# Kernel optimization log

Measured on AMD Instinct MI355X. Metric: run time of the kernel, lower is better.

Reference implementation:

```python
import jax, jax.numpy as jnp
import numpy as np

B, T, C, H = 2, 2048, 1024, 16
D = C // H  # head dim = 64
EPS = 1e-5


def setup_inputs() -> dict:
    key = jax.random.key(0)
    k1, k2, k3 = jax.random.split(key, 3)
    x = jax.random.normal(k1, (B, T, C), dtype=jnp.float32)
    W_attn = jax.random.normal(k2, (3 * C, C), dtype=jnp.float32) * 0.02
    W_proj = jax.random.normal(k3, (C, C), dtype=jnp.float32) * 0.02
    # standard RoPE inverse frequencies, one per rotation pair (D//2)
    rope_freqs = 1.0 / (10000.0 ** (jnp.arange(D // 2, dtype=jnp.float32) * 2.0 / D))
    ln_weight = jnp.ones((C,), dtype=jnp.float32)
    ln_bias = jnp.zeros((C,), dtype=jnp.float32)
    return {"x": x, "rope_freqs": rope_freqs, "W_attn": W_attn,
            "W_proj": W_proj, "ln_weight": ln_weight, "ln_bias": ln_bias}


def _apply_rope(q, k, freqs):
    # q,k: [B,H,S,D]; matches torch apply_rope: split even/odd, concat halves
    S = q.shape[-2]
    theta = jnp.arange(S, dtype=q.dtype)[:, None] * freqs[None, :]  # [S, D/2]
    sin_t, cos_t = jnp.sin(theta), jnp.cos(theta)

    def rot(t):
        t1, t2 = t[..., 0::2], t[..., 1::2]
        return jnp.concatenate([t1 * cos_t - t2 * sin_t,
                                t1 * sin_t + t2 * cos_t], axis=-1)

    return rot(q), rot(k)


def reference(x, rope_freqs, W_attn, W_proj, ln_weight, ln_bias):
    Bv, Tv, Cv = x.shape
    qkv = x @ W_attn.T                      # [B,T,3C] (F.linear, no bias)
    q, k, v = jnp.split(qkv, 3, axis=-1)
    resh = lambda t: t.reshape(Bv, Tv, H, D).transpose(0, 2, 1, 3)  # [B,H,T,D]
    q, k, v = resh(q), resh(k), resh(v)
    q, k = _apply_rope(q, k, rope_freqs)
    scale = 1.0 / jnp.sqrt(jnp.asarray(D, dtype=x.dtype))
    scores = jnp.einsum('bhqd,bhkd->bhqk', q, k) * scale
    causal = jnp.tril(jnp.ones((Tv, Tv), dtype=bool))
    scores = jnp.where(causal[None, None], scores, -jnp.inf)
    att = jax.nn.softmax(scores, axis=-1)
    y = jnp.einsum('bhqk,bhkd->bhqd', att, v)
    y = y.transpose(0, 2, 1, 3).reshape(Bv, Tv, Cv)
    y = y @ W_proj.T                        # c_proj (bias=False)
    # resid dropout is identity in eval; LayerNorm (eps=1e-5, biased var)
    mean = jnp.mean(y, axis=-1, keepdims=True)
    var = jnp.mean(jnp.square(y - mean), axis=-1, keepdims=True)
    return (y - mean) / jnp.sqrt(var + EPS) * ln_weight + ln_bias
```

## Files before the change

kernel.cpp:

```cpp
#include <hip/hip_runtime.h>
#include <hip/hip_bf16.h>
#include <math.h>

typedef short bf16x8 __attribute__((ext_vector_type(8)));
typedef float f32x4 __attribute__((ext_vector_type(4)));

#define T_SEQ 2048
#define C_DIM 1024
#define H_HEADS 16
#define D_HEAD 64
#define BT 4096
#define C3 3072
#define BH 32

static __device__ inline unsigned short bf_bits(float f) {
    __hip_bfloat16 h = __float2bfloat16(f);
    unsigned short u;
    __builtin_memcpy(&u, &h, 2);
    return u;
}

static __device__ inline unsigned int cvtpk(float lo, float hi) {
    unsigned int r;
    asm("v_cvt_pk_bf16_f32 %0, %1, %2" : "=v"(r) : "v"(lo), "v"(hi));
    return r;
}

__device__ __forceinline__ void gload16(const void* g, void* l) {
    __builtin_amdgcn_global_load_lds(
        (const __attribute__((address_space(1))) void*)g,
        (__attribute__((address_space(3))) void*)l, 16, 0, 0);
}

__device__ __forceinline__ int swz(int r) {
    return ((((r & 3) ^ ((r >> 3) & 3)) | (((r >> 3) & 1) << 2)) << 3);
}

__global__ void cast_f32_bf16(const float* __restrict__ in,
                              __hip_bfloat16* __restrict__ out, int n4) {
    int i = blockIdx.x * blockDim.x + threadIdx.x;
    if (i >= n4) return;
    float4 v = reinterpret_cast<const float4*>(in)[i];
    ushort4 o;
    o.x = bf_bits(v.x); o.y = bf_bits(v.y); o.z = bf_bits(v.z); o.w = bf_bits(v.w);
    reinterpret_cast<ushort4*>(out)[i] = o;
}

template<int OUT_BF16>
__global__ __launch_bounds__(256) void gemm_bt(
    const __hip_bfloat16* __restrict__ A,
    const __hip_bfloat16* __restrict__ Bw,
    void* __restrict__ Cout, int M, int N, int K) {
    __shared__ __hip_bfloat16 As[2][128][64];
    __shared__ __hip_bfloat16 Bs[2][128][64];
    const int t = threadIdx.x;
    const int lane = t & 63, w = t >> 6;
    const int wr = w >> 1, wc = w & 1;
    const int l15 = lane & 15, lg = lane >> 4;
    const int m0 = blockIdx.y * 128, n0 = blockIdx.x * 128;

    const int srow = lane >> 3;
    const int scol = ((lane & 7) ^ srow) * 8;
    const int xr = (l15 & 7) << 3;

    f32x4 acc[4][4];
    f32x4 zero4 = {0.f, 0.f, 0.f, 0.f};
#pragma unroll
    for (int m = 0; m < 4; m++)
#pragma unroll
        for (int n = 0; n < 4; n++) acc[m][n] = zero4;

    auto stage = [&](int buf, int k0) {
#pragma unroll
        for (int i = 0; i < 4; i++) {
            int rbase = w * 32 + i * 8;
            gload16(&A[(size_t)(m0 + rbase + srow) * K + k0 + scol], &As[buf][rbase][0]);
            gload16(&Bw[(size_t)(n0 + rbase + srow) * K + k0 + scol], &Bs[buf][rbase][0]);
        }
    };

    const int nt = K >> 6;
    stage(0, 0);
    __syncthreads();

    for (int tk = 0; tk < nt; tk++) {
        const int cur = tk & 1;
        if (tk + 1 < nt) stage(cur ^ 1, (tk + 1) << 6);
#pragma unroll
        for (int kk = 0; kk < 2; kk++) {
            bf16x8 a[4], b[4];
            const int co = (kk * 32 + lg * 8) ^ xr;
#pragma unroll
            for (int m = 0; m < 4; m++)
                a[m] = *reinterpret_cast<const bf16x8*>(&As[cur][wr * 64 + m * 16 + l15][co]);
#pragma unroll
            for (int n = 0; n < 4; n++)
                b[n] = *reinterpret_cast<const bf16x8*>(&Bs[cur][wc * 64 + n * 16 + l15][co]);
            __builtin_amdgcn_s_setprio(1);
#pragma unroll
            for (int m = 0; m < 4; m++)
#pragma unroll
                for (int n = 0; n < 4; n++)
                    acc[m][n] = __builtin_amdgcn_mfma_f32_16x16x32_bf16(a[m], b[n], acc[m][n], 0, 0, 0);
            __builtin_amdgcn_s_setprio(0);
        }
        __syncthreads();
    }

#pragma unroll
    for (int m = 0; m < 4; m++)
#pragma unroll
        for (int n = 0; n < 4; n++)
#pragma unroll
            for (int jj = 0; jj < 4; jj++) {
                int row = m0 + wr * 64 + m * 16 + lg * 4 + jj;
                int col = n0 + wc * 64 + n * 16 + l15;
                float v = acc[m][n][jj];
                if (OUT_BF16)
                    ((__hip_bfloat16*)Cout)[(size_t)row * N + col] = __float2bfloat16(v);
                else
                    ((float*)Cout)[(size_t)row * N + col] = v;
            }
}

__global__ void rope_qk(const __hip_bfloat16* __restrict__ qkv,
                        const float* __restrict__ freqs,
                        __hip_bfloat16* __restrict__ q_s,
                        __hip_bfloat16* __restrict__ k_s) {
    int idx = blockIdx.x * 256 + threadIdx.x;
    int i = idx & 31;
    int h = (idx >> 5) & 15;
    int bt = idx >> 9;
    int b = bt >> 11;
    int tp = bt & 2047;
    float th = (float)tp * freqs[i];
    float sn = sinf(th), cs = cosf(th);
    size_t qoff = (size_t)bt * C3 + h * 64;
    float q1 = __bfloat162float(qkv[qoff + 2 * i]);
    float q2 = __bfloat162float(qkv[qoff + 2 * i + 1]);
    float k1 = __bfloat162float(qkv[qoff + C_DIM + 2 * i]);
    float k2 = __bfloat162float(qkv[qoff + C_DIM + 2 * i + 1]);
    size_t obase = ((size_t)(b * H_HEADS + h) * T_SEQ + tp) * D_HEAD;
    const float sc = 0.125f * 1.44269504f;
    q_s[obase + i]      = __float2bfloat16((q1 * cs - q2 * sn) * sc);
    q_s[obase + 32 + i] = __float2bfloat16((q1 * sn + q2 * cs) * sc);
    k_s[obase + i]      = __float2bfloat16(k1 * cs - k2 * sn);
    k_s[obase + 32 + i] = __float2bfloat16(k1 * sn + k2 * cs);
}

__global__ __launch_bounds__(256) void transpose_v(const __hip_bfloat16* __restrict__ qkv,
                                                   __hip_bfloat16* __restrict__ v_t) {
    __shared__ __hip_bfloat16 tile[64][72];
    const int bh = blockIdx.y, tt = blockIdx.x;
    const int b = bh >> 4, h = bh & 15;
    const int t = threadIdx.x;
    const int r = t >> 2, c0 = (t & 3) * 16;
    const __hip_bfloat16* src = qkv + (size_t)(b * T_SEQ + tt * 64 + r) * C3 + 2 * C_DIM + h * 64 + c0;
    uint4 v0 = reinterpret_cast<const uint4*>(src)[0];
    uint4 v1 = reinterpret_cast<const uint4*>(src)[1];
    *reinterpret_cast<uint4*>(&tile[r][c0]) = v0;
    *reinterpret_cast<uint4*>(&tile[r][c0 + 8]) = v1;
    __syncthreads();
    const int d = t >> 2;
    ushort out[16];
#pragma unroll
    for (int i = 0; i < 16; i++) {
        __hip_bfloat16 x = tile[c0 + i][d];
        __builtin_memcpy(&out[i], &x, 2);
    }
    __hip_bfloat16* dst = v_t + (size_t)bh * D_HEAD * T_SEQ + (size_t)d * T_SEQ + tt * 64 + c0;
    reinterpret_cast<uint4*>(dst)[0] = *reinterpret_cast<uint4*>(&out[0]);
    reinterpret_cast<uint4*>(dst)[1] = *reinterpret_cast<uint4*>(&out[8]);
}

__global__ __launch_bounds__(256, 4) void attn_kernel(
    const __hip_bfloat16* __restrict__ q_s,
    const __hip_bfloat16* __restrict__ k_s,
    const __hip_bfloat16* __restrict__ v_t,
    __hip_bfloat16* __restrict__ y) {
    __shared__ ushort Kbuf[2][64 * 64];
    __shared__ ushort Vbuf[2][64 * 64];

    const int bid = blockIdx.x;
    const int qt = 31 - (bid >> 5);
    const int bh = bid & 31;
    const int t = threadIdx.x, lane = t & 63, w = t >> 6;
    const int l15 = lane & 15, lg = lane >> 4;
    const size_t hbase = (size_t)bh * T_SEQ * D_HEAD;
    const int qr = qt * 64 + w * 16 + l15;

    bf16x8 aq[2];
#pragma unroll
    for (int dd = 0; dd < 2; dd++)
        aq[dd] = *reinterpret_cast<const bf16x8*>(&q_s[hbase + (size_t)qr * 64 + dd * 32 + lg * 8]);

    bf16x8 ones;
#pragma unroll
    for (int i = 0; i < 8; i++) ones[i] = (short)0x3F80;

    f32x4 zero4 = {0.f, 0.f, 0.f, 0.f};
    f32x4 o[4];
#pragma unroll
    for (int dc = 0; dc < 4; dc++) o[dc] = zero4;
    f32x4 lacc = zero4;
    float mr = -INFINITY;

    int koff[4][2], voff[4][2];
#pragma unroll
    for (int c = 0; c < 4; c++) {
        int kro = ((c >> 1) << 5) + ((c & 1) << 2) + ((l15 >> 2) << 3) + (l15 & 3);
        int sz = swz(kro);
#pragma unroll
        for (int dd = 0; dd < 2; dd++)
            koff[c][dd] = kro * 64 + ((dd * 32 + lg * 8) ^ sz);
    }
#pragma unroll
    for (int dc = 0; dc < 4; dc++) {
        int vro = dc * 16 + l15;
        int sz = swz(vro);
#pragma unroll
        for (int dd = 0; dd < 2; dd++)
            voff[dc][dd] = vro * 64 + ((dd * 32 + lg * 8) ^ sz);
    }

    const int srow = t >> 3;
    const int sgr = t & 7;

    auto stageKV = [&](int buf, int kbase) {
#pragma unroll
        for (int i = 0; i < 2; i++) {
            int r = i * 32 + srow;
            int gsw = (sgr ^ (swz(r) >> 3)) * 8;
            gload16(&k_s[hbase + (size_t)(kbase + r) * 64 + gsw],
                    &Kbuf[buf][(i * 32 + w * 8) * 64]);
            gload16(&v_t[hbase + (size_t)r * T_SEQ + kbase + gsw],
                    &Vbuf[buf][(i * 32 + w * 8) * 64]);
        }
    };

    int cur = 0;
    stageKV(0, 0);
    __syncthreads();

    for (int kt = 0; kt <= qt; kt++) {
        const int kt64 = kt << 6;
        if (kt < qt) stageKV(cur ^ 1, kt64 + 64);

        const ushort* Kc = Kbuf[cur];
        const ushort* Vc = Vbuf[cur];
        bf16x8 kf[4][2], av[4][2];
#pragma unroll
        for (int c = 0; c < 4; c++)
#pragma unroll
            for (int dd = 0; dd < 2; dd++)
                kf[c][dd] = *reinterpret_cast<const bf16x8*>(&Kc[koff[c][dd]]);
#pragma unroll
        for (int dc = 0; dc < 4; dc++)
#pragma unroll
            for (int dd = 0; dd < 2; dd++)
                av[dc][dd] = *reinterpret_cast<const bf16x8*>(&Vc[voff[dc][dd]]);

        f32x4 st[4];
        __builtin_amdgcn_s_setprio(1);
#pragma unroll
        for (int c = 0; c < 4; c++) {
            st[c] = zero4;
#pragma unroll
            for (int dd = 0; dd < 2; dd++)
                st[c] = __builtin_amdgcn_mfma_f32_16x16x32_bf16(kf[c][dd], aq[dd], st[c], 0, 0, 0);
        }
        __builtin_amdgcn_s_setprio(0);

        if (kt == qt) {
#pragma unroll
            for (int c = 0; c < 4; c++) {
                int kb = kt64 + ((c >> 1) << 5) + ((c & 1) << 2) + lg * 8;
#pragma unroll
                for (int jj = 0; jj < 4; jj++)
                    if (kb + jj > qr) st[c][jj] = -INFINITY;
            }
        }

        float m0a = fmaxf(st[0][0], st[0][1]), m0b = fmaxf(st[0][2], st[0][3]);
        float m1a = fmaxf(st[1][0], st[1][1]), m1b = fmaxf(st[1][2], st[1][3]);
        float m2a = fmaxf(st[2][0], st[2][1]), m2b = fmaxf(st[2][2], st[2][3]);
        float m3a = fmaxf(st[3][0], st[3][1]), m3b = fmaxf(st[3][2], st[3][3]);
        float mx = fmaxf(fmaxf(fmaxf(m0a, m0b), fmaxf(m1a, m1b)),
                         fmaxf(fmaxf(m2a, m2b), fmaxf(m3a, m3b)));
        mx = fmaxf(mx, __shfl_xor(mx, 16));
        mx = fmaxf(mx, __shfl_xor(mx, 32));

        if (__any(mx - mr > 8.f)) {
            float mnew = fmaxf(mr, mx);
            float scl = __builtin_amdgcn_exp2f(mr - mnew);
            mr = mnew;
            lacc[0] *= scl;
#pragma unroll
            for (int dc = 0; dc < 4; dc++)
#pragma unroll
                for (int jj = 0; jj < 4; jj++) o[dc][jj] *= scl;
        }

#pragma unroll
        for (int c = 0; c < 4; c++)
#pragma unroll
            for (int jj = 0; jj < 4; jj++)
                st[c][jj] = __builtin_amdgcn_exp2f(st[c][jj] - mr);

        union { bf16x8 v; unsigned int u[4]; } pf0, pf1;
        pf0.u[0] = cvtpk(st[0][0], st[0][1]);
        pf0.u[1] = cvtpk(st[0][2], st[0][3]);
        pf0.u[2] = cvtpk(st[1][0], st[1][1]);
        pf0.u[3] = cvtpk(st[1][2], st[1][3]);
        pf1.u[0] = cvtpk(st[2][0], st[2][1]);
        pf1.u[1] = cvtpk(st[2][2], st[2][3]);
        pf1.u[2] = cvtpk(st[3][0], st[3][1]);
        pf1.u[3] = cvtpk(st[3][2], st[3][3]);

        __builtin_amdgcn_s_setprio(1);
        lacc = __builtin_amdgcn_mfma_f32_16x16x32_bf16(ones, pf0.v, lacc, 0, 0, 0);
        lacc = __builtin_amdgcn_mfma_f32_16x16x32_bf16(ones, pf1.v, lacc, 0, 0, 0);
#pragma unroll
        for (int dc = 0; dc < 4; dc++) {
            o[dc] = __builtin_amdgcn_mfma_f32_16x16x32_bf16(av[dc][0], pf0.v, o[dc], 0, 0, 0);
            o[dc] = __builtin_amdgcn_mfma_f32_16x16x32_bf16(av[dc][1], pf1.v, o[dc], 0, 0, 0);
        }
        __builtin_amdgcn_s_setprio(0);

        __syncthreads();
        cur ^= 1;
    }

    const int b = bh >> 4, h = bh & 15;
    float inv = 1.f / lacc[0];
#pragma unroll
    for (int dc = 0; dc < 4; dc++) {
        ushort4 ov;
        ov.x = bf_bits(o[dc][0] * inv);
        ov.y = bf_bits(o[dc][1] * inv);
        ov.z = bf_bits(o[dc][2] * inv);
        ov.w = bf_bits(o[dc][3] * inv);
        *reinterpret_cast<ushort4*>(
            &y[(size_t)(b * T_SEQ + qr) * C_DIM + h * 64 + dc * 16 + lg * 4]) = ov;
    }
}

__global__ __launch_bounds__(256) void ln_kernel(const __hip_bfloat16* __restrict__ y2,
                                                 const float* __restrict__ wgt,
                                                 const float* __restrict__ bias,
                                                 float* __restrict__ out) {
    const int row = blockIdx.x;
    const int t = threadIdx.x;
    ushort4 u = reinterpret_cast<const ushort4*>(y2 + (size_t)row * C_DIM)[t];
    float4 v;
    v.x = __bfloat162float(*(__hip_bfloat16*)&u.x);
    v.y = __bfloat162float(*(__hip_bfloat16*)&u.y);
    v.z = __bfloat162float(*(__hip_bfloat16*)&u.z);
    v.w = __bfloat162float(*(__hip_bfloat16*)&u.w);
    float s = v.x + v.y + v.z + v.w;
    float s2 = v.x * v.x + v.y * v.y + v.z * v.z + v.w * v.w;
#pragma unroll
    for (int d = 1; d < 64; d <<= 1) {
        s += __shfl_xor(s, d);
        s2 += __shfl_xor(s2, d);
    }
    __shared__ float ps[4], ps2[4];
    const int lane = t & 63, w = t >> 6;
    if (lane == 0) { ps[w] = s; ps2[w] = s2; }
    __syncthreads();
    s = ps[0] + ps[1] + ps[2] + ps[3];
    s2 = ps2[0] + ps2[1] + ps2[2] + ps2[3];
    float mean = s * (1.f / C_DIM);
    float var = s2 * (1.f / C_DIM) - mean * mean;
    float inv = rsqrtf(var + 1e-5f);
    float4 wv = reinterpret_cast<const float4*>(wgt)[t];
    float4 bv = reinterpret_cast<const float4*>(bias)[t];
    float4 ov;
    ov.x = (v.x - mean) * inv * wv.x + bv.x;
    ov.y = (v.y - mean) * inv * wv.y + bv.y;
    ov.z = (v.z - mean) * inv * wv.z + bv.z;
    ov.w = (v.w - mean) * inv * wv.w + bv.w;
    reinterpret_cast<float4*>(out + (size_t)row * C_DIM)[t] = ov;
}

extern "C" void kernel_launch(void* const* d_in, const int* in_sizes, int n_in,
                              void* d_out, int out_size, void* d_ws, size_t ws_size,
                              hipStream_t stream) {
    const float* x      = (const float*)d_in[0];
    const float* freqs  = (const float*)d_in[1];
    const float* W_attn = (const float*)d_in[2];
    const float* W_proj = (const float*)d_in[3];
    const float* lnw    = (const float*)d_in[4];
    const float* lnb    = (const float*)d_in[5];
    float* out = (float*)d_out;
    char* ws = (char*)d_ws;

    __hip_bfloat16* xb   = (__hip_bfloat16*)(ws);
    __hip_bfloat16* Wab  = (__hip_bfloat16*)(ws + 8388608);
    __hip_bfloat16* Wpb  = (__hip_bfloat16*)(ws + 14680064);
    __hip_bfloat16* qkvb = (__hip_bfloat16*)(ws + 16777216);
    __hip_bfloat16* q_s  = (__hip_bfloat16*)(ws + 41943040);
    __hip_bfloat16* k_s  = (__hip_bfloat16*)(ws + 50331648);
    __hip_bfloat16* v_t  = (__hip_bfloat16*)(ws + 58720256);
    __hip_bfloat16* y_at = (__hip_bfloat16*)(ws + 67108864);
    __hip_bfloat16* y2b  = (__hip_bfloat16*)(ws + 75497472);

    cast_f32_bf16<<<(BT * C_DIM / 4) / 256, 256, 0, stream>>>(x, xb, BT * C_DIM / 4);
    cast_f32_bf16<<<(C3 * C_DIM / 4) / 256, 256, 0, stream>>>(W_attn, Wab, C3 * C_DIM / 4);
    cast_f32_bf16<<<(C_DIM * C_DIM / 4) / 256, 256, 0, stream>>>(W_proj, Wpb, C_DIM * C_DIM / 4);

    gemm_bt<1><<<dim3(C3 / 128, BT / 128), 256, 0, stream>>>(xb, Wab, qkvb, BT, C3, C_DIM);

    rope_qk<<<(BT * H_HEADS * 32) / 256, 256, 0, stream>>>(qkvb, freqs, q_s, k_s);
    transpose_v<<<dim3(T_SEQ / 64, BH), 256, 0, stream>>>(qkvb, v_t);

    attn_kernel<<<1024, 256, 0, stream>>>(q_s, k_s, v_t, y_at);

    gemm_bt<1><<<dim3(C_DIM / 128, BT / 128), 256, 0, stream>>>(y_at, Wpb, y2b, BT, C_DIM, C_DIM);

    ln_kernel<<<BT, 256, 0, stream>>>(y2b, lnw, lnb, out);
}
```

Baseline: 127.6 us.

## Use partial vmcnt waits for double-buffered loads and swizzle GEMM block order

Replaces the __syncthreads calls in the GEMM and attention main loops with explicit s_waitcnt vmcnt(N) plus s_barrier. Each iteration waits only for the current buffer's async global-to-LDS loads, so the prefetch of the next tile stays in flight while the MFMAs run. The GEMM also remaps workgroup IDs in groups of 8, which is meant to spread neighbouring blocks across XCDs and improve L2 locality. The trade-off is that correctness now depends on the vmcnt constants exactly matching the number of issued loads per stage, and the remap assumes the workgroup count is divisible by 8.

New measurement: 128.6 us. No clear change (+0.8%).

```diff
diff --git a/kernel.cpp b/kernel.cpp
--- a/kernel.cpp
+++ b/kernel.cpp
@@ -35,6 +35,17 @@
 __device__ __forceinline__ int swz(int r) {
     return ((((r & 3) ^ ((r >> 3) & 3)) | (((r >> 3) & 1) << 2)) << 3);
 }
+
+#define PIPE_WAIT_BARRIER(N)                                   \
+    asm volatile("s_waitcnt vmcnt(" #N ")" ::: "memory");      \
+    __builtin_amdgcn_s_barrier();                              \
+    asm volatile("" ::: "memory");                             \
+    __builtin_amdgcn_sched_barrier(0)
+
+#define PIPE_END_BARRIER()                                     \
+    asm volatile("" ::: "memory");                             \
+    __builtin_amdgcn_sched_barrier(0);                         \
+    __builtin_amdgcn_s_barrier()
 
 __global__ void cast_f32_bf16(const float* __restrict__ in,
                               __hip_bfloat16* __restrict__ out, int n4) {
@@ -57,7 +68,13 @@
     const int lane = t & 63, w = t >> 6;
     const int wr = w >> 1, wc = w & 1;
     const int l15 = lane & 15, lg = lane >> 4;
-    const int m0 = blockIdx.y * 128, n0 = blockIdx.x * 128;
+
+    const int gx = gridDim.x;
+    const int nwg = gx * gridDim.y;
+    const int orig = blockIdx.x + gx * blockIdx.y;
+    const int cpx = nwg >> 3;
+    const int wg = (orig & 7) * cpx + (orig >> 3);
+    const int m0 = (wg / gx) * 128, n0 = (wg % gx) * 128;
 
     const int srow = lane >> 3;
     const int scol = ((lane & 7) ^ srow) * 8;
@@ -81,11 +98,15 @@
 
     const int nt = K >> 6;
     stage(0, 0);
-    __syncthreads();
+    int cur = 0;
 
     for (int tk = 0; tk < nt; tk++) {
-        const int cur = tk & 1;
-        if (tk + 1 < nt) stage(cur ^ 1, (tk + 1) << 6);
+        if (tk + 1 < nt) {
+            stage(cur ^ 1, (tk + 1) << 6);
+            PIPE_WAIT_BARRIER(8);
+        } else {
+            PIPE_WAIT_BARRIER(0);
+        }
 #pragma unroll
         for (int kk = 0; kk < 2; kk++) {
             bf16x8 a[4], b[4];
@@ -104,7 +125,8 @@
                     acc[m][n] = __builtin_amdgcn_mfma_f32_16x16x32_bf16(a[m], b[n], acc[m][n], 0, 0, 0);
             __builtin_amdgcn_s_setprio(0);
         }
-        __syncthreads();
+        PIPE_END_BARRIER();
+        cur ^= 1;
     }
 
 #pragma unroll
@@ -240,11 +262,15 @@
 
     int cur = 0;
     stageKV(0, 0);
-    __syncthreads();
 
     for (int kt = 0; kt <= qt; kt++) {
         const int kt64 = kt << 6;
-        if (kt < qt) stageKV(cur ^ 1, kt64 + 64);
+        if (kt < qt) {
+            stageKV(cur ^ 1, kt64 + 64);
+            PIPE_WAIT_BARRIER(4);
+        } else {
+            PIPE_WAIT_BARRIER(0);
+        }
 
         const ushort* Kc = Kbuf[cur];
         const ushort* Vc = Vbuf[cur];
@@ -327,7 +353,7 @@
         }
         __builtin_amdgcn_s_setprio(0);
 
-        __syncthreads();
+        PIPE_END_BARRIER();
         cur ^= 1;
     }
 
```
